# Kernel optimization log

Measured on AMD Instinct MI355X. Metric: run time of the kernel, lower is better.

The kernel has to match this reference:

```python
import jax, jax.numpy as jnp
import numpy as np

X_SIZE, NUM_NEURONS, Z_SIZE = 2048, 4096, 64
D = X_SIZE + NUM_NEURONS + Z_SIZE  # 6208
TOPK, ZTOPK = 16, 8
EPS_TIE = 1e-9
RND = 0.5  # stand-in for random.random(); tie indicator t is 0 w.p. 1 for continuous inputs


def setup_inputs() -> dict:
    key = jax.random.key(0)
    k1, k2, k3, k4, k5 = jax.random.split(key, 5)
    x = jax.random.normal(k1, (X_SIZE,), dtype=jnp.float32)
    z = jax.random.normal(k2, (Z_SIZE,), dtype=jnp.float32)
    y_response = jax.random.uniform(k3, (NUM_NEURONS,), dtype=jnp.float32)
    neurons = jax.random.normal(k4, (D, D), dtype=jnp.float32)
    ages = 1.0 + 9.0 * jax.random.uniform(k5, (D,), dtype=jnp.float32)  # ages >= 1
    return {"x": x, "z": z, "y_response": y_response, "neurons": neurons, "ages": ages}


def _update_rows(neurons, ages, inpt, idx, vals):
    # Faithful to update_neuron_weights, including the (1,k)@(k,D) row-mix
    # that broadcasts the same mixed row to all k winner rows.
    a = ages[idx]                                   # (k,)
    upd = (vals / a)[:, None] * inpt[None, :]       # (k, D)
    mix = jnp.einsum('k,kd->d', (a - 1.0) / a, neurons[idx])  # (D,)
    new_rows = mix[None, :] + upd                   # (k, D)
    norm = jnp.sqrt(jnp.sum(new_rows * new_rows, axis=1, keepdims=True)) + 1e-12
    neurons = neurons.at[idx].set(new_rows / norm)
    ages = ages.at[idx].add(1.0)
    return neurons, ages


def reference(x, z, y_response, neurons, ages):
    # Steady-state path: num_neurons_init == max_num_neurons (> topk),
    # supervized_z = supervized_x = None, xtopk = None.
    x0, x1 = 0, X_SIZE
    y0, y1 = X_SIZE, X_SIZE + NUM_NEURONS
    z0 = X_SIZE + NUM_NEURONS

    inpt = jnp.concatenate([x, y_response, z])      # (D,)
    response = neurons @ inpt                       # (D,)
    final = jnp.zeros_like(response)

    # --- z path: top-(ztopk) winners, normalized against runner-up ---
    zvals, zidx = jax.lax.top_k(response[z0:], ZTOPK + 1)
    gz = z0 + zidx
    final = final.at[gz[:-1]].set((zvals[:-1] - zvals[-1]) / (zvals[0] - zvals[-1]))
    neurons, ages = _update_rows(neurons, ages, inpt, gz[:-1], zvals[:-1])

    # --- x path (xtopk None, unsupervised): normalize full x response ---
    rx = response[x0:x1]
    tx = jnp.where(jnp.all(rx == 0.0), 1.0, 0.0)
    xvals = rx / (jnp.max(rx) + EPS_TIE * tx * RND)
    final = final.at[x0:x1].set(xvals)
    xidx = jnp.arange(x0, x1)
    neurons, ages = _update_rows(neurons, ages, inpt, xidx[:-1], xvals[:-1])

    # --- y path: fully grown net -> topk winner-take-most branch ---
    yvals, yidx = jax.lax.top_k(response[y0:y1], TOPK + 1)
    gy = y0 + yidx
    ty = jnp.where(jnp.any(yvals[:-1] == yvals[-1]), 1.0, 0.0)
    final = final.at[gy[:-1]].set(
        (yvals[:-1] - yvals[-1]) / (yvals[0] - yvals[-1] + EPS_TIE * ty * RND))
    neurons, ages = _update_rows(neurons, ages, inpt, gy[:-1], yvals[:-1])

    z_response = final[z0:]
    return z_response, final, neurons, ages
```

## Files before the change

kernel.cpp:

```cpp
#include <hip/hip_runtime.h>
#include <math.h>

typedef float v4f __attribute__((ext_vector_type(4)));

#define XS 2048
#define NN 4096
#define ZS 64
#define DD 6208
#define D4 1552
#define Z0 (XS + NN)
#define TOPK 16
#define ZTOPK 8
#define EPS_TIE 1e-9f
#define RNDC 0.5f
#define NXUPD 2047

#define OUT_FINAL 64
#define OUT_NEUR  (64 + DD)
#define OUT_AGES  (OUT_NEUR + (size_t)DD * DD)

#define WS_RESP   0
#define WS_INPT   DD
#define WS_MIXX   (2 * DD)
#define WS_MIXZ   (3 * DD)
#define WS_MIXY   (4 * DD)
#define WS_SCAL   (5 * DD)
#define WS_SELROW (WS_SCAL + 32)
#define WS_SELC   (WS_SELROW + 24)
#define WS_SELW   (WS_SELC + 24)
#define WS_TOTAL  (WS_SELW + 32)

#define XBLKS 1024
#define CSPL  388
#define YZBLKS (DD - XS)
#define AUXBLKS 11

#define RBLKS 388

__device__ __forceinline__ v4f ld4(const float* p) { return *(const v4f*)p; }
__device__ __forceinline__ v4f v4z() { v4f v; v.x = v.y = v.z = v.w = 0.f; return v; }
__device__ __forceinline__ float dot4(v4f a, v4f b) {
  return fmaf(a.x, b.x, fmaf(a.y, b.y, fmaf(a.z, b.z, a.w * b.w)));
}
__device__ __forceinline__ v4f load_inpt(const float* x, const float* yr,
                                         const float* zv, int c) {
  int col = c * 4;
  if (col < XS) return ld4(x + col);
  if (col < Z0) return ld4(yr + (col - XS));
  return ld4(zv + (col - Z0));
}
__device__ __forceinline__ v4f wred4(v4f a) {
  #pragma unroll
  for (int m = 32; m >= 1; m >>= 1) {
    a.x += __shfl_xor(a.x, m); a.y += __shfl_xor(a.y, m);
    a.z += __shfl_xor(a.z, m); a.w += __shfl_xor(a.w, m);
  }
  return a;
}

__global__ __launch_bounds__(256) void k_phase1(
    const float* __restrict__ x, const float* __restrict__ yr,
    const float* __restrict__ zv, const float* __restrict__ neurons,
    const float* __restrict__ ages, float* __restrict__ ws,
    float* __restrict__ out)
{
  const int t = threadIdx.x;
  const int b = blockIdx.x;
  float* outn = out + OUT_NEUR;

  if (b < XBLKS) {
    const int rg = b >> 2, cs = b & 3;
    const int row0 = rg * 8;
    const int cbase = cs * CSPL;
    const int c0 = cbase + t;
    const int c1 = cbase + 256 + t;
    const bool has1 = (t < CSPL - 256);

    v4f i0 = load_inpt(x, yr, zv, c0);
    v4f i1 = has1 ? load_inpt(x, yr, zv, c1) : v4z();
    if (b < 4) {
      ((v4f*)(ws + WS_INPT))[c0] = i0;
      if (has1) ((v4f*)(ws + WS_INPT))[c1] = i1;
    }

    float wr[8];
    #pragma unroll
    for (int r = 0; r < 8; ++r) {
      float a = ages[row0 + r];
      wr[r] = (row0 + r < NXUPD) ? (a - 1.f) / a : 0.f;
    }

    float dot[8];
    v4f m0 = v4z(), m1 = v4z();
    #pragma unroll
    for (int r = 0; r < 8; ++r) {
      const int row = row0 + r;
      const float* rp = neurons + (size_t)row * DD;
      v4f a0 = ld4(rp + 4 * c0);
      v4f a1 = has1 ? ld4(rp + 4 * c1) : v4z();
      dot[r] = dot4(a0, i0) + dot4(a1, i1);
      m0 += wr[r] * a0;
      m1 += wr[r] * a1;
      if (row >= NXUPD) {
        __builtin_nontemporal_store(a0, (v4f*)(outn + (size_t)row * DD + 4 * c0));
        if (has1)
          __builtin_nontemporal_store(a1, (v4f*)(outn + (size_t)row * DD + 4 * c1));
      }
    }

    __shared__ float wred[4][8];
    const int lane = t & 63, wv = t >> 6;
    #pragma unroll
    for (int r = 0; r < 8; ++r) {
      float v = dot[r];
      #pragma unroll
      for (int m = 32; m >= 1; m >>= 1) v += __shfl_xor(v, m);
      if (lane == 0) wred[wv][r] = v;
    }
    __syncthreads();
    if (t < 8)
      atomicAdd(ws + WS_RESP + row0 + t,
                wred[0][t] + wred[1][t] + wred[2][t] + wred[3][t]);

    float* pm = outn + (size_t)rg * DD;
    *(v4f*)(pm + 4 * c0) = m0;
    if (has1) *(v4f*)(pm + 4 * c1) = m1;
  } else if (b < XBLKS + YZBLKS) {
    const int row = 2048 + (b - XBLKS);
    const float* rp = neurons + (size_t)row * DD;
    float* op = outn + (size_t)row * DD;
    float dot = 0.f;
    #pragma unroll
    for (int k = 0; k < 6; ++k) {
      const int c = t + 256 * k;
      v4f a = ld4(rp + 4 * c);
      v4f iv = load_inpt(x, yr, zv, c);
      dot += dot4(a, iv);
      __builtin_nontemporal_store(a, (v4f*)(op + 4 * c));
    }
    if (t < 16) {
      const int c = 1536 + t;
      v4f a = ld4(rp + 4 * c);
      v4f iv = ld4(zv + (4 * c - Z0));
      dot += dot4(a, iv);
      __builtin_nontemporal_store(a, (v4f*)(op + 4 * c));
    }
    __shared__ float red[4];
    const int lane = t & 63, wv = t >> 6;
    #pragma unroll
    for (int m = 32; m >= 1; m >>= 1) dot += __shfl_xor(dot, m);
    if (lane == 0) red[wv] = dot;
    __syncthreads();
    if (t == 0) ws[WS_RESP + row] = red[0] + red[1] + red[2] + red[3];
  } else {
    const int e = b - (XBLKS + YZBLKS);
    const int base = e * 1024;
    #pragma unroll
    for (int k = 0; k < 4; ++k) {
      int j = base + t + 256 * k;
      if (j < DD) {
        out[OUT_AGES + j] = ages[j] + ((j < NXUPD) ? 1.f : 0.f);
      } else {
        int f = j - DD;
        if (f < DD - XS) out[OUT_FINAL + XS + f] = 0.f;
      }
    }
  }
}

__global__ __launch_bounds__(1024) void k_phase2(
    const float* __restrict__ ages, float* __restrict__ ws, float* __restrict__ out)
{
  const int t = threadIdx.x;
  const int lane = t & 63, wv = t >> 6;
  __shared__ float s_candv[16 * (TOPK + 1)];
  __shared__ int   s_candi[16 * (TOPK + 1)];
  __shared__ float s_zval[ZTOPK + 1];
  __shared__ int   s_zidx[ZTOPK + 1];
  __shared__ float s_yval[TOPK + 1];
  __shared__ int   s_yidx[TOPK + 1];
  __shared__ float s_red[16];
  __shared__ int   s_redi[16];
  __shared__ float s_denx, s_ty;

  float* resp = ws + WS_RESP;
  float* fin  = out + OUT_FINAL;
  float* oag  = out + OUT_AGES;

  {
    float v0 = resp[t], v1 = resp[t + 1024];
    float lm = fmaxf(v0, v1);
    int nz = (v0 != 0.f) | (v1 != 0.f);
    #pragma unroll
    for (int m = 1; m < 64; m <<= 1) { lm = fmaxf(lm, __shfl_xor(lm, m)); nz |= __shfl_xor(nz, m); }
    if (lane == 0) { s_red[wv] = lm; s_redi[wv] = nz; }
  }

  {
    float v[4]; int id[4];
    #pragma unroll
    for (int q = 0; q < 4; ++q) { int i = (wv << 8) + (q << 6) + lane; id[q] = i; v[q] = resp[XS + i]; }
    for (int j = 0; j <= TOPK; ++j) {
      float bv = v[0]; int bi = id[0];
      #pragma unroll
      for (int q = 1; q < 4; ++q)
        if (v[q] > bv || (v[q] == bv && id[q] < bi)) { bv = v[q]; bi = id[q]; }
      #pragma unroll
      for (int m = 1; m < 64; m <<= 1) {
        float ov = __shfl_xor(bv, m); int oi = __shfl_xor(bi, m);
        if (ov > bv || (ov == bv && oi < bi)) { bv = ov; bi = oi; }
      }
      if (lane == 0) { s_candv[wv * (TOPK + 1) + j] = bv; s_candi[wv * (TOPK + 1) + j] = bi; }
      #pragma unroll
      for (int q = 0; q < 4; ++q) if (id[q] == bi) v[q] = -INFINITY;
    }
  }

  if (wv == 0) {
    float v = resp[Z0 + lane];
    for (int j = 0; j <= ZTOPK; ++j) {
      float bv = v; int bi = lane;
      #pragma unroll
      for (int m = 1; m < 64; m <<= 1) {
        float ov = __shfl_xor(bv, m); int oi = __shfl_xor(bi, m);
        if (ov > bv || (ov == bv && oi < bi)) { bv = ov; bi = oi; }
      }
      if (lane == 0) { s_zval[j] = bv; s_zidx[j] = bi; }
      if (lane == bi) v = -INFINITY;
    }
  }

  __syncthreads();

  if (t == 64) {
    float m2 = -INFINITY; int n2 = 0;
    for (int q = 0; q < 16; ++q) { m2 = fmaxf(m2, s_red[q]); n2 |= s_redi[q]; }
    float dx = m2 + EPS_TIE * (n2 ? 0.f : 1.f) * RNDC;
    s_denx = dx;
    ws[WS_SCAL + 7] = dx;
  }
  if (wv == 0) {
    float mv[5]; int mi[5];
    #pragma unroll
    for (int q = 0; q < 5; ++q) {
      int k = lane + (q << 6);
      if (k < 16 * (TOPK + 1)) { mv[q] = s_candv[k]; mi[q] = s_candi[k]; }
      else { mv[q] = -INFINITY; mi[q] = 0x7fffffff; }
    }
    for (int j = 0; j <= TOPK; ++j) {
      float bv = mv[0]; int bi = mi[0];
      #pragma unroll
      for (int q = 1; q < 5; ++q)
        if (mv[q] > bv || (mv[q] == bv && mi[q] < bi)) { bv = mv[q]; bi = mi[q]; }
      #pragma unroll
      for (int m = 1; m < 64; m <<= 1) {
        float ov = __shfl_xor(bv, m); int oi = __shfl_xor(bi, m);
        if (ov > bv || (ov == bv && oi < bi)) { bv = ov; bi = oi; }
      }
      if (lane == 0) { s_yval[j] = bv; s_yidx[j] = bi; }
      #pragma unroll
      for (int q = 0; q < 5; ++q) if (mi[q] == bi) mv[q] = -INFINITY;
    }
    if (lane == 0) {
      float ty = 0.f;
      for (int q = 0; q < TOPK; ++q) if (s_yval[q] == s_yval[TOPK]) ty = 1.f;
      s_ty = ty;
    }
  }
  __syncthreads();

  const float denx  = s_denx;
  fin[t]        = resp[t] / denx;
  fin[t + 1024] = resp[t + 1024] / denx;

  const float zlast = s_zval[ZTOPK];
  const float zden  = s_zval[0] - zlast;
  const float ylast = s_yval[TOPK];
  const float yden  = s_yval[0] - ylast + EPS_TIE * s_ty * RNDC;

  if (t < ZTOPK) {
    int zi = s_zidx[t];
    int row = Z0 + zi;
    fin[row] = (s_zval[t] - zlast) / zden;
    float a = ages[row];
    ((int*)(ws + WS_SELROW))[t] = row;
    ws[WS_SELC + t] = s_zval[t] / a;
    ws[WS_SELW + t] = (a - 1.f) / a;
    oag[row] = a + 1.f;
  } else if (t >= 32 && t < 32 + TOPK) {
    int k = t - 32;
    int row = XS + s_yidx[k];
    fin[row] = (s_yval[k] - ylast) / yden;
    float a = ages[row];
    ((int*)(ws + WS_SELROW))[ZTOPK + k] = row;
    ws[WS_SELC + ZTOPK + k] = s_yval[k] / a;
    ws[WS_SELW + ZTOPK + k] = (a - 1.f) / a;
    oag[row] = a + 1.f;
  } else if (t >= 128 && t < 192) {
    int i = t - 128;
    float v = 0.f;
    for (int k = 0; k < ZTOPK; ++k) if (s_zidx[k] == i) v = (s_zval[k] - zlast) / zden;
    out[i] = v;
  }
}

__global__ __launch_bounds__(256) void k_phase3a(
    const float* __restrict__ neurons, const float* __restrict__ outn,
    float* __restrict__ ws)
{
  const int b = blockIdx.x;
  const int t = threadIdx.x;
  if (b < ZTOPK + TOPK) {
    const int row = ((const int*)(ws + WS_SELROW))[b];
    const float w = ws[WS_SELW + b];
    float* dst = ws + ((b < ZTOPK) ? WS_MIXZ : WS_MIXY);
    const float* src = neurons + (size_t)row * DD;
    #pragma unroll
    for (int k = 0; k < 6; ++k) {
      const int c = t + 256 * k;
      v4f a = ld4(src + 4 * c);
      atomicAdd(dst + 4 * c + 0, w * a.x);
      atomicAdd(dst + 4 * c + 1, w * a.y);
      atomicAdd(dst + 4 * c + 2, w * a.z);
      atomicAdd(dst + 4 * c + 3, w * a.w);
    }
    if (t < 16) {
      const int c = 1536 + t;
      v4f a = ld4(src + 4 * c);
      atomicAdd(dst + 4 * c + 0, w * a.x);
      atomicAdd(dst + 4 * c + 1, w * a.y);
      atomicAdd(dst + 4 * c + 2, w * a.z);
      atomicAdd(dst + 4 * c + 3, w * a.w);
    }
  } else {
    const int g = b - (ZTOPK + TOPK);
    const int cb = 4 * g;
    const float* pr = outn + (size_t)t * DD + 4 * cb;
    v4f a0 = ld4(pr), a1 = ld4(pr + 4), a2 = ld4(pr + 8), a3 = ld4(pr + 12);
    a0 = wred4(a0); a1 = wred4(a1); a2 = wred4(a2); a3 = wred4(a3);
    __shared__ v4f sred[4][4];
    if ((t & 63) == 0) {
      int w = t >> 6;
      sred[w][0] = a0; sred[w][1] = a1; sred[w][2] = a2; sred[w][3] = a3;
    }
    __syncthreads();
    if (t < 4) {
      v4f s = sred[0][t] + sred[1][t] + sred[2][t] + sred[3][t];
      *(v4f*)(ws + WS_MIXX + 4 * (cb + t)) = s;
    }
  }
}

__global__ __launch_bounds__(1024) void k_phase3b(float* __restrict__ ws)
{
  const int t = threadIdx.x;
  __shared__ float red[16][7];
  const float* inpt = ws + WS_INPT;
  float s0 = 0.f, s1 = 0.f, s2 = 0.f, s3 = 0.f, s4 = 0.f, s5 = 0.f, s6 = 0.f;
  for (int i = t; i < DD; i += 1024) {
    float ip = inpt[i];
    float mx = ws[WS_MIXX + i], mz = ws[WS_MIXZ + i], my = ws[WS_MIXY + i];
    s0 = fmaf(ip, ip, s0);
    s1 = fmaf(mx, mx, s1); s2 = fmaf(mx, ip, s2);
    s3 = fmaf(mz, mz, s3); s4 = fmaf(mz, ip, s4);
    s5 = fmaf(my, my, s5); s6 = fmaf(my, ip, s6);
  }
  #pragma unroll
  for (int m = 1; m < 64; m <<= 1) {
    s0 += __shfl_xor(s0, m); s1 += __shfl_xor(s1, m); s2 += __shfl_xor(s2, m);
    s3 += __shfl_xor(s3, m); s4 += __shfl_xor(s4, m); s5 += __shfl_xor(s5, m);
    s6 += __shfl_xor(s6, m);
  }
  if ((t & 63) == 0) {
    int w = t >> 6;
    red[w][0] = s0; red[w][1] = s1; red[w][2] = s2; red[w][3] = s3;
    red[w][4] = s4; red[w][5] = s5; red[w][6] = s6;
  }
  __syncthreads();
  if (t == 0) {
    float a[7] = {0.f, 0.f, 0.f, 0.f, 0.f, 0.f, 0.f};
    for (int q = 0; q < 16; ++q)
      for (int k = 0; k < 7; ++k) a[k] += red[q][k];
    float* scal = ws + WS_SCAL;
    for (int k = 0; k < 7; ++k) scal[k] = a[k];
  }
}

__global__ __launch_bounds__(256) void k_phase4(
    const float* __restrict__ ages, const float* __restrict__ ws,
    float* __restrict__ outn)
{
  const int b = blockIdx.x;
  const int t = threadIdx.x;
  const float sii = ws[WS_SCAL + 0];
  int row; float c, smm, smi; const float* mix;
  if (b < NXUPD) {
    row = b;
    float a = ages[row];
    c = (ws[WS_RESP + row] / ws[WS_SCAL + 7]) / a;
    mix = ws + WS_MIXX; smm = ws[WS_SCAL + 1]; smi = ws[WS_SCAL + 2];
  } else {
    int k = b - NXUPD;
    row = ((const int*)(ws + WS_SELROW))[k];
    c = ws[WS_SELC + k];
    if (k < ZTOPK) { mix = ws + WS_MIXZ; smm = ws[WS_SCAL + 3]; smi = ws[WS_SCAL + 4]; }
    else           { mix = ws + WS_MIXY; smm = ws[WS_SCAL + 5]; smi = ws[WS_SCAL + 6]; }
  }
  const float inv = 1.f / (sqrtf(fmaf(c, fmaf(c, sii, 2.f * smi), smm)) + 1e-12f);
  const float* inpt = ws + WS_INPT;
  float* dst = outn + (size_t)row * DD;
  #pragma unroll
  for (int k = 0; k < 6; ++k) {
    const int i = t + 256 * k;
    v4f m4 = ((const v4f*)(mix))[i];
    v4f i4 = ((const v4f*)(inpt))[i];
    v4f o = (m4 + c * i4) * inv;
    __builtin_nontemporal_store(o, (v4f*)dst + i);
  }
  if (t < 16) {
    const int i = 1536 + t;
    v4f m4 = ((const v4f*)(mix))[i];
    v4f i4 = ((const v4f*)(inpt))[i];
    v4f o = (m4 + c * i4) * inv;
    __builtin_nontemporal_store(o, (v4f*)dst + i);
  }
}

extern "C" void kernel_launch(void* const* d_in, const int* in_sizes, int n_in,
                              void* d_out, int out_size, void* d_ws, size_t ws_size,
                              hipStream_t stream)
{
  (void)in_sizes; (void)n_in; (void)out_size; (void)ws_size;
  const float* x    = (const float*)d_in[0];
  const float* zin  = (const float*)d_in[1];
  const float* yr   = (const float*)d_in[2];
  const float* neur = (const float*)d_in[3];
  const float* ages = (const float*)d_in[4];
  float* out = (float*)d_out;
  float* ws  = (float*)d_ws;

  hipMemsetAsync(d_ws, 0, (size_t)WS_TOTAL * sizeof(float), stream);
  k_phase1<<<XBLKS + YZBLKS + AUXBLKS, 256, 0, stream>>>(x, yr, zin, neur, ages, ws, out);
  k_phase2<<<1, 1024, 0, stream>>>(ages, ws, out);
  k_phase3a<<<ZTOPK + TOPK + RBLKS, 256, 0, stream>>>(neur, out + OUT_NEUR, ws);
  k_phase3b<<<1, 1024, 0, stream>>>(ws);
  k_phase4<<<NXUPD + ZTOPK + TOPK, 256, 0, stream>>>(ages, ws, out + OUT_NEUR);
}
```

Measured before the change: 321.0 us.

## Remove memset and atomics, fuse phase3 kernels, batch loads for memory parallelism

Phase 1 now writes per-column-split partial dot products to separate slots instead of using atomicAdd into a zeroed buffer, which removes the need for hipMemsetAsync. Phase 3a and 3b are merged into one kernel. The z/y mix rows are computed per column with register accumulation instead of scalar atomics, and the norm scalars are accumulated into 64 padded slots that phase 4 reduces. Loads in phase 1 are hoisted into arrays so more memory requests are in flight, and launch bounds request higher occupancy. The cost is more registers, extra partial-sum reads, and a redundant 7x64 reduction in every phase-4 block.

```diff
diff --git a/kernel.cpp b/kernel.cpp
--- a/kernel.cpp
+++ b/kernel.cpp
@@ -19,16 +19,19 @@
 #define OUT_NEUR  (64 + DD)
 #define OUT_AGES  (OUT_NEUR + (size_t)DD * DD)
 
-#define WS_RESP   0
-#define WS_INPT   DD
-#define WS_MIXX   (2 * DD)
-#define WS_MIXZ   (3 * DD)
-#define WS_MIXY   (4 * DD)
-#define WS_SCAL   (5 * DD)
-#define WS_SELROW (WS_SCAL + 32)
-#define WS_SELC   (WS_SELROW + 24)
-#define WS_SELW   (WS_SELC + 24)
-#define WS_TOTAL  (WS_SELW + 32)
+#define WS_RESP    0
+#define WS_RESPP   DD
+#define WS_INPT    (DD + 8192)
+#define WS_MIXX    (WS_INPT + DD)
+#define WS_MIXZ    (WS_MIXX + DD)
+#define WS_MIXY    (WS_MIXZ + DD)
+#define WS_SCAL    (WS_MIXY + DD)
+#define WS_SCALPAD (WS_SCAL + 32)
+#define WS_SELROW  (WS_SCALPAD + 448)
+#define WS_SELC    (WS_SELROW + 24)
+#define WS_SELW    (WS_SELC + 24)
+#define WS_TOTAL   (WS_SELW + 32)
+
 
 #define XBLKS 1024
 #define CSPL  388
@@ -36,6 +39,7 @@
 #define AUXBLKS 11
 
 #define RBLKS 388
+#define GBLKS 16
 
 __device__ __forceinline__ v4f ld4(const float* p) { return *(const v4f*)p; }
 __device__ __forceinline__ v4f v4z() { v4f v; v.x = v.y = v.z = v.w = 0.f; return v; }
@@ -58,7 +62,7 @@
   return a;
 }
 
-__global__ __launch_bounds__(256) void k_phase1(
+__global__ __launch_bounds__(256, 4) void k_phase1(
     const float* __restrict__ x, const float* __restrict__ yr,
     const float* __restrict__ zv, const float* __restrict__ neurons,
     const float* __restrict__ ages, float* __restrict__ ws,
@@ -90,22 +94,26 @@
       wr[r] = (row0 + r < NXUPD) ? (a - 1.f) / a : 0.f;
     }
 
+    v4f a0[8], a1[8];
+    #pragma unroll
+    for (int r = 0; r < 8; ++r)
+      a0[r] = ld4(neurons + (size_t)(row0 + r) * DD + 4 * c0);
+    #pragma unroll
+    for (int r = 0; r < 8; ++r)
+      a1[r] = has1 ? ld4(neurons + (size_t)(row0 + r) * DD + 4 * c1) : v4z();
+
     float dot[8];
     v4f m0 = v4z(), m1 = v4z();
     #pragma unroll
     for (int r = 0; r < 8; ++r) {
-      const int row = row0 + r;
-      const float* rp = neurons + (size_t)row * DD;
-      v4f a0 = ld4(rp + 4 * c0);
-      v4f a1 = has1 ? ld4(rp + 4 * c1) : v4z();
-      dot[r] = dot4(a0, i0) + dot4(a1, i1);
-      m0 += wr[r] * a0;
-      m1 += wr[r] * a1;
-      if (row >= NXUPD) {
-        __builtin_nontemporal_store(a0, (v4f*)(outn + (size_t)row * DD + 4 * c0));
-        if (has1)
-          __builtin_nontemporal_store(a1, (v4f*)(outn + (size_t)row * DD + 4 * c1));
-      }
+      dot[r] = dot4(a0[r], i0) + dot4(a1[r], i1);
+      m0 += wr[r] * a0[r];
+      m1 += wr[r] * a1[r];
+    }
+    if (row0 + 7 >= NXUPD) {
+      __builtin_nontemporal_store(a0[7], (v4f*)(outn + (size_t)2047 * DD + 4 * c0));
+      if (has1)
+        __builtin_nontemporal_store(a1[7], (v4f*)(outn + (size_t)2047 * DD + 4 * c1));
     }
 
     __shared__ float wred[4][8];
@@ -119,8 +127,8 @@
     }
     __syncthreads();
     if (t < 8)
-      atomicAdd(ws + WS_RESP + row0 + t,
-                wred[0][t] + wred[1][t] + wred[2][t] + wred[3][t]);
+      ws[WS_RESPP + cs * 2048 + row0 + t] =
+          wred[0][t] + wred[1][t] + wred[2][t] + wred[3][t];
 
     float* pm = outn + (size_t)rg * DD;
     *(v4f*)(pm + 4 * c0) = m0;
@@ -129,21 +137,25 @@
     const int row = 2048 + (b - XBLKS);
     const float* rp = neurons + (size_t)row * DD;
     float* op = outn + (size_t)row * DD;
+
+    v4f a[6], iv[6];
+    #pragma unroll
+    for (int k = 0; k < 6; ++k) a[k] = ld4(rp + 4 * (t + 256 * k));
+    #pragma unroll
+    for (int k = 0; k < 6; ++k) iv[k] = load_inpt(x, yr, zv, t + 256 * k);
+
     float dot = 0.f;
     #pragma unroll
     for (int k = 0; k < 6; ++k) {
-      const int c = t + 256 * k;
-      v4f a = ld4(rp + 4 * c);
-      v4f iv = load_inpt(x, yr, zv, c);
-      dot += dot4(a, iv);
-      __builtin_nontemporal_store(a, (v4f*)(op + 4 * c));
+      dot += dot4(a[k], iv[k]);
+      __builtin_nontemporal_store(a[k], (v4f*)op + (t + 256 * k));
     }
     if (t < 16) {
       const int c = 1536 + t;
-      v4f a = ld4(rp + 4 * c);
-      v4f iv = ld4(zv + (4 * c - Z0));
-      dot += dot4(a, iv);
-      __builtin_nontemporal_store(a, (v4f*)(op + 4 * c));
+      v4f ae = ld4(rp + 4 * c);
+      v4f ie = ld4(zv + (4 * c - Z0));
+      dot += dot4(ae, ie);
+      __builtin_nontemporal_store(ae, (v4f*)op + c);
     }
     __shared__ float red[4];
     const int lane = t & 63, wv = t >> 6;
@@ -173,6 +185,7 @@
 {
   const int t = threadIdx.x;
   const int lane = t & 63, wv = t >> 6;
+  __shared__ float s_xsum[XS];
   __shared__ float s_candv[16 * (TOPK + 1)];
   __shared__ int   s_candi[16 * (TOPK + 1)];
   __shared__ float s_zval[ZTOPK + 1];
@@ -187,8 +200,16 @@
   float* fin  = out + OUT_FINAL;
   float* oag  = out + OUT_AGES;
 
+  if (t < 448) ws[WS_SCALPAD + t] = 0.f;
+
   {
-    float v0 = resp[t], v1 = resp[t + 1024];
+    float v0 = 0.f, v1 = 0.f;
+    #pragma unroll
+    for (int cs = 0; cs < 4; ++cs) {
+      v0 += ws[WS_RESPP + cs * 2048 + t];
+      v1 += ws[WS_RESPP + cs * 2048 + t + 1024];
+    }
+    s_xsum[t] = v0; s_xsum[t + 1024] = v1;
     float lm = fmaxf(v0, v1);
     int nz = (v0 != 0.f) | (v1 != 0.f);
     #pragma unroll
@@ -270,8 +291,8 @@
   __syncthreads();
 
   const float denx  = s_denx;
-  fin[t]        = resp[t] / denx;
-  fin[t + 1024] = resp[t + 1024] / denx;
+  fin[t]        = s_xsum[t] / denx;
+  fin[t + 1024] = s_xsum[t + 1024] / denx;
 
   const float zlast = s_zval[ZTOPK];
   const float zden  = s_zval[0] - zlast;
@@ -304,41 +325,20 @@
   }
 }
 
-__global__ __launch_bounds__(256) void k_phase3a(
+__global__ __launch_bounds__(256, 4) void k_phase3(
     const float* __restrict__ neurons, const float* __restrict__ outn,
     float* __restrict__ ws)
 {
   const int b = blockIdx.x;
   const int t = threadIdx.x;
-  if (b < ZTOPK + TOPK) {
-    const int row = ((const int*)(ws + WS_SELROW))[b];
-    const float w = ws[WS_SELW + b];
-    float* dst = ws + ((b < ZTOPK) ? WS_MIXZ : WS_MIXY);
-    const float* src = neurons + (size_t)row * DD;
-    #pragma unroll
-    for (int k = 0; k < 6; ++k) {
-      const int c = t + 256 * k;
-      v4f a = ld4(src + 4 * c);
-      atomicAdd(dst + 4 * c + 0, w * a.x);
-      atomicAdd(dst + 4 * c + 1, w * a.y);
-      atomicAdd(dst + 4 * c + 2, w * a.z);
-      atomicAdd(dst + 4 * c + 3, w * a.w);
-    }
-    if (t < 16) {
-      const int c = 1536 + t;
-      v4f a = ld4(src + 4 * c);
-      atomicAdd(dst + 4 * c + 0, w * a.x);
-      atomicAdd(dst + 4 * c + 1, w * a.y);
-      atomicAdd(dst + 4 * c + 2, w * a.z);
-      atomicAdd(dst + 4 * c + 3, w * a.w);
-    }
-  } else {
-    const int g = b - (ZTOPK + TOPK);
-    const int cb = 4 * g;
+
+  if (b < RBLKS) {
+    const int cb = 4 * b;
     const float* pr = outn + (size_t)t * DD + 4 * cb;
     v4f a0 = ld4(pr), a1 = ld4(pr + 4), a2 = ld4(pr + 8), a3 = ld4(pr + 12);
     a0 = wred4(a0); a1 = wred4(a1); a2 = wred4(a2); a3 = wred4(a3);
     __shared__ v4f sred[4][4];
+    __shared__ float sp[4][3];
     if ((t & 63) == 0) {
       int w = t >> 6;
       sred[w][0] = a0; sred[w][1] = a1; sred[w][2] = a2; sred[w][3] = a3;
@@ -347,64 +347,101 @@
     if (t < 4) {
       v4f s = sred[0][t] + sred[1][t] + sred[2][t] + sred[3][t];
       *(v4f*)(ws + WS_MIXX + 4 * (cb + t)) = s;
-    }
-  }
-}
-
-__global__ __launch_bounds__(1024) void k_phase3b(float* __restrict__ ws)
-{
-  const int t = threadIdx.x;
-  __shared__ float red[16][7];
-  const float* inpt = ws + WS_INPT;
-  float s0 = 0.f, s1 = 0.f, s2 = 0.f, s3 = 0.f, s4 = 0.f, s5 = 0.f, s6 = 0.f;
-  for (int i = t; i < DD; i += 1024) {
-    float ip = inpt[i];
-    float mx = ws[WS_MIXX + i], mz = ws[WS_MIXZ + i], my = ws[WS_MIXY + i];
-    s0 = fmaf(ip, ip, s0);
-    s1 = fmaf(mx, mx, s1); s2 = fmaf(mx, ip, s2);
-    s3 = fmaf(mz, mz, s3); s4 = fmaf(mz, ip, s4);
-    s5 = fmaf(my, my, s5); s6 = fmaf(my, ip, s6);
-  }
-  #pragma unroll
-  for (int m = 1; m < 64; m <<= 1) {
-    s0 += __shfl_xor(s0, m); s1 += __shfl_xor(s1, m); s2 += __shfl_xor(s2, m);
-    s3 += __shfl_xor(s3, m); s4 += __shfl_xor(s4, m); s5 += __shfl_xor(s5, m);
-    s6 += __shfl_xor(s6, m);
-  }
-  if ((t & 63) == 0) {
-    int w = t >> 6;
-    red[w][0] = s0; red[w][1] = s1; red[w][2] = s2; red[w][3] = s3;
-    red[w][4] = s4; red[w][5] = s5; red[w][6] = s6;
-  }
-  __syncthreads();
-  if (t == 0) {
-    float a[7] = {0.f, 0.f, 0.f, 0.f, 0.f, 0.f, 0.f};
-    for (int q = 0; q < 16; ++q)
-      for (int k = 0; k < 7; ++k) a[k] += red[q][k];
-    float* scal = ws + WS_SCAL;
-    for (int k = 0; k < 7; ++k) scal[k] = a[k];
-  }
-}
-
-__global__ __launch_bounds__(256) void k_phase4(
+      v4f ip = ld4(ws + WS_INPT + 4 * (cb + t));
+      sp[t][0] = dot4(ip, ip);
+      sp[t][1] = dot4(s, s);
+      sp[t][2] = dot4(s, ip);
+    }
+    __syncthreads();
+    if (t == 0) {
+      const int slot = b & 63;
+      #pragma unroll
+      for (int k = 0; k < 3; ++k) {
+        float p = sp[0][k] + sp[1][k] + sp[2][k] + sp[3][k];
+        atomicAdd(ws + WS_SCALPAD + k * 64 + slot, p);
+      }
+    }
+  } else {
+    const int g = b - RBLKS;
+    const int c = 97 * g + t;
+    const int* selr = (const int*)(ws + WS_SELROW);
+    float p0 = 0.f, p1 = 0.f, p2 = 0.f, p3 = 0.f;
+    if (t < 97) {
+      v4f mz = v4z(), my = v4z();
+      #pragma unroll
+      for (int k = 0; k < ZTOPK; ++k) {
+        const int row = selr[k];
+        const float w = ws[WS_SELW + k];
+        mz += w * ld4(neurons + (size_t)row * DD + 4 * c);
+      }
+      #pragma unroll
+      for (int k = ZTOPK; k < ZTOPK + TOPK; ++k) {
+        const int row = selr[k];
+        const float w = ws[WS_SELW + k];
+        my += w * ld4(neurons + (size_t)row * DD + 4 * c);
+      }
+      *(v4f*)(ws + WS_MIXZ + 4 * c) = mz;
+      *(v4f*)(ws + WS_MIXY + 4 * c) = my;
+      v4f ip = ld4(ws + WS_INPT + 4 * c);
+      p0 = dot4(mz, mz); p1 = dot4(mz, ip);
+      p2 = dot4(my, my); p3 = dot4(my, ip);
+    }
+    #pragma unroll
+    for (int m = 1; m < 64; m <<= 1) {
+      p0 += __shfl_xor(p0, m); p1 += __shfl_xor(p1, m);
+      p2 += __shfl_xor(p2, m); p3 += __shfl_xor(p3, m);
+    }
+    __shared__ float gr[4][4];
+    if ((t & 63) == 0) {
+      int w = t >> 6;
+      gr[w][0] = p0; gr[w][1] = p1; gr[w][2] = p2; gr[w][3] = p3;
+    }
+    __syncthreads();
+    if (t == 0) {
+      const int slot = b & 63;
+      #pragma unroll
+      for (int k = 0; k < 4; ++k) {
+        float p = gr[0][k] + gr[1][k] + gr[2][k] + gr[3][k];
+        atomicAdd(ws + WS_SCALPAD + (3 + k) * 64 + slot, p);
+      }
+    }
+  }
+}
+
+__global__ __launch_bounds__(256, 4) void k_phase4(
     const float* __restrict__ ages, const float* __restrict__ ws,
     float* __restrict__ outn)
 {
   const int b = blockIdx.x;
   const int t = threadIdx.x;
-  const float sii = ws[WS_SCAL + 0];
+
+  __shared__ float s_scal[7];
+  if (t < 64) {
+    #pragma unroll
+    for (int k = 0; k < 7; ++k) {
+      float v = ws[WS_SCALPAD + k * 64 + t];
+      #pragma unroll
+      for (int m = 1; m < 64; m <<= 1) v += __shfl_xor(v, m);
+      if (t == 0) s_scal[k] = v;
+    }
+  }
+  __syncthreads();
+
+  const float sii = s_scal[0];
   int row; float c, smm, smi; const float* mix;
   if (b < NXUPD) {
     row = b;
     float a = ages[row];
-    c = (ws[WS_RESP + row] / ws[WS_SCAL + 7]) / a;
-    mix = ws + WS_MIXX; smm = ws[WS_SCAL + 1]; smi = ws[WS_SCAL + 2];
+    float rsum = ws[WS_RESPP + row] + ws[WS_RESPP + 2048 + row] +
+                 ws[WS_RESPP + 4096 + row] + ws[WS_RESPP + 6144 + row];
+    c = (rsum / ws[WS_SCAL + 7]) / a;
+    mix = ws + WS_MIXX; smm = s_scal[1]; smi = s_scal[2];
   } else {
     int k = b - NXUPD;
     row = ((const int*)(ws + WS_SELROW))[k];
     c = ws[WS_SELC + k];
-    if (k < ZTOPK) { mix = ws + WS_MIXZ; smm = ws[WS_SCAL + 3]; smi = ws[WS_SCAL + 4]; }
-    else           { mix = ws + WS_MIXY; smm = ws[WS_SCAL + 5]; smi = ws[WS_SCAL + 6]; }
+    if (k < ZTOPK) { mix = ws + WS_MIXZ; smm = s_scal[3]; smi = s_scal[4]; }
+    else           { mix = ws + WS_MIXY; smm = s_scal[5]; smi = s_scal[6]; }
   }
   const float inv = 1.f / (sqrtf(fmaf(c, fmaf(c, sii, 2.f * smi), smm)) + 1e-12f);
   const float* inpt = ws + WS_INPT;
@@ -439,10 +476,8 @@
   float* out = (float*)d_out;
   float* ws  = (float*)d_ws;
 
-  hipMemsetAsync(d_ws, 0, (size_t)WS_TOTAL * sizeof(float), stream);
   k_phase1<<<XBLKS + YZBLKS + AUXBLKS, 256, 0, stream>>>(x, yr, zin, neur, ages, ws, out);
   k_phase2<<<1, 1024, 0, stream>>>(ages, ws, out);
-  k_phase3a<<<ZTOPK + TOPK + RBLKS, 256, 0, stream>>>(neur, out + OUT_NEUR, ws);
-  k_phase3b<<<1, 1024, 0, stream>>>(ws);
+  k_phase3<<<RBLKS + GBLKS, 256, 0, stream>>>(neur, out + OUT_NEUR, ws);
   k_phase4<<<NXUPD + ZTOPK + TOPK, 256, 0, stream>>>(ages, ws, out + OUT_NEUR);
 }
```

Result: no change. 317.6 us (-1.1%).
